# Kernel optimization log

Measured on AMD Instinct MI355X. Metric: run time of the kernel, lower is better.

Reference implementation:

```python
import jax, jax.numpy as jnp
import numpy as np
from jax import lax

WIN = (9, 9, 9)
EPS = 1e-05


def _sum1d(x, axis, win):
    """Sliding-window sum of size `win` along `axis`, zero-padded (SAME)."""
    pad = win // 2
    pads = [(pad, pad) if a == axis else (0, 0) for a in range(x.ndim)]
    xp = jnp.pad(x, pads)
    c = jnp.cumsum(xp, axis=axis)
    c = jnp.pad(c, [(1, 0) if a == axis else (0, 0) for a in range(x.ndim)])
    n = x.shape[axis]
    return (lax.slice_in_dim(c, win, win + n, axis=axis)
            - lax.slice_in_dim(c, 0, n, axis=axis))


def _box_sum(x):
    """Separable 3D box-filter sum == conv3d with ones([9,9,9]), SAME pad."""
    for axis, w in zip((2, 3, 4), WIN):
        x = _sum1d(x, axis, w)
    return x


def setup_inputs() -> dict:
    key = jax.random.key(0)
    k1, k2 = jax.random.split(key)
    shape = (2, 1, 128, 128, 128)
    y_pred = jax.random.normal(k1, shape, dtype=jnp.float32)
    y_true = jax.random.normal(k2, shape, dtype=jnp.float32)
    return {"y_pred": y_pred, "y_true": y_true}


def reference(y_pred, y_true):
    I = y_true.astype(jnp.float32)
    J = y_pred.astype(jnp.float32)
    win_size = float(np.prod(WIN))  # 729

    I_sum = _box_sum(I)
    J_sum = _box_sum(J)
    I2_sum = _box_sum(I * I)
    J2_sum = _box_sum(J * J)
    IJ_sum = _box_sum(I * J)

    u_I = I_sum / win_size
    u_J = J_sum / win_size

    cross = IJ_sum - u_J * I_sum - u_I * J_sum + u_I * u_J * win_size
    I_var = I2_sum - 2 * u_I * I_sum + u_I * u_I * win_size
    J_var = J2_sum - 2 * u_J * J_sum + u_J * u_J * win_size

    cc_map = cross * cross / (I_var * J_var + EPS)
    return jnp.mean(-cc_map)
```

## Files before the change

### kernel.cpp

```cpp
#include <hip/hip_runtime.h>

#define DSZ 128
#define NVOX 4194304.0f

__global__ void ncc_zero(float* out) { out[0] = 0.0f; }

__device__ __forceinline__ float4 f4add(const float4 a, const float4 b) {
    return make_float4(a.x + b.x, a.y + b.y, a.z + b.z, a.w + b.w);
}
__device__ __forceinline__ float4 f4sub(const float4 a, const float4 b) {
    return make_float4(a.x - b.x, a.y - b.y, a.z - b.z, a.w - b.w);
}

__global__ __launch_bounds__(256, 2) void ncc_main(const float* __restrict__ Iin,
                                                   const float* __restrict__ Jin,
                                                   float* __restrict__ out)
{
    const int tx0 = blockIdx.x * 16;
    const int ty0 = blockIdx.y * 32;
    const int b   = blockIdx.z >> 3;
    const int tz0 = (blockIdx.z & 7) * 16;
    const int tid = threadIdx.x;
    const int lx  = tid & 15;
    const int ys  = tid >> 4;

    const float* __restrict__ Ib = Iin + b * (DSZ * DSZ * DSZ);
    const float* __restrict__ Jb = Jin + b * (DSZ * DSZ * DSZ);

    __shared__ float4 s4m[4][40][17];
    __shared__ float  s1v[4][40][24];

    float4 rA4[8], rB4[8];
    float  rA1[8], rB1[8];
#pragma unroll
    for (int i = 0; i < 8; ++i) {
        rA4[i] = make_float4(0.f, 0.f, 0.f, 0.f); rB4[i] = rA4[i];
        rA1[i] = 0.f; rB1[i] = 0.f;
    }
    float4 zA4 = make_float4(0.f, 0.f, 0.f, 0.f), zB4 = zA4;
    float  zA1 = 0.f, zB1 = 0.f;
    float  acc = 0.f;

    auto emit_cc = [&](const float4& z4, const float z1) {
        const float inv = 1.0f / 729.0f;
        const float uI = z4.x * inv;
        const float uJ = z4.y * inv;
        const float cross = z1 - uJ * z4.x - uI * z4.y + uI * uJ * 729.0f;
        const float Ivar  = z4.z - 2.0f * uI * z4.x + uI * uI * 729.0f;
        const float Jvar  = z4.w - 2.0f * uJ * z4.y + uJ * uJ * 729.0f;
        acc += cross * cross / (Ivar * Jvar + 1e-5f);
    };

#pragma unroll 1
    for (int mr = 0; mr < 3; ++mr) {
#pragma unroll
        for (int r4 = 0; r4 < 4; ++r4) {
            const int rnd = 4 * mr + r4;

            for (int t = tid; t < 320; t += 256) {
                const int p   = (t >= 160);
                const int t2  = t - 160 * p;
                const int r   = t2 >> 2;
                const int xg  = t2 & 3;
                const int zp  = tz0 + 2 * rnd + p - 4;
                const int gy  = ty0 + r - 4;
                const int gxb = tx0 + 4 * xg - 4;
                const bool ok = ((unsigned)zp < (unsigned)DSZ) &&
                                ((unsigned)gy < (unsigned)DSZ);
                const int zoff = (zp * DSZ + gy) * DSZ;

                float vi[12], vj[12];
#pragma unroll
                for (int g = 0; g < 3; ++g) {
                    const int gx = gxb + 4 * g;
                    float4 va = make_float4(0.f, 0.f, 0.f, 0.f);
                    float4 vb = va;
                    if (ok && (unsigned)gx < (unsigned)DSZ) {
                        va = *(const float4*)(Ib + zoff + gx);
                        vb = *(const float4*)(Jb + zoff + gx);
                    }
                    vi[4*g+0]=va.x; vi[4*g+1]=va.y; vi[4*g+2]=va.z; vi[4*g+3]=va.w;
                    vj[4*g+0]=vb.x; vj[4*g+1]=vb.y; vj[4*g+2]=vb.z; vj[4*g+3]=vb.w;
                }

                float wI=0.f, wJ=0.f, wII=0.f, wJJ=0.f, wIJ=0.f;
#pragma unroll
                for (int k = 0; k < 9; ++k) {
                    wI += vi[k]; wJ += vj[k];
                    wII = fmaf(vi[k], vi[k], wII);
                    wJJ = fmaf(vj[k], vj[k], wJJ);
                    wIJ = fmaf(vi[k], vj[k], wIJ);
                }
                const int sl = (r4 & 1) * 2 + p;
                float mIJ[4];
                s4m[sl][r][4*xg] = make_float4(wI, wJ, wII, wJJ);
                mIJ[0] = wIJ;
#pragma unroll
                for (int j = 1; j < 4; ++j) {
                    const float ai = vi[8+j], aj = vj[8+j];
                    const float di = vi[j-1], dj = vj[j-1];
                    wI += ai - di; wJ += aj - dj;
                    wII += fmaf(ai, ai, -di * di);
                    wJJ += fmaf(aj, aj, -dj * dj);
                    wIJ += fmaf(ai, aj, -di * dj);
                    s4m[sl][r][4*xg + j] = make_float4(wI, wJ, wII, wJJ);
                    mIJ[j] = wIJ;
                }
                *(float4*)&s1v[sl][r][4*xg] = make_float4(mIJ[0], mIJ[1], mIJ[2], mIJ[3]);
            }
            __syncthreads();

#pragma unroll
            for (int p = 0; p < 2; ++p) {
                const int sl = (r4 & 1) * 2 + p;
                float4 c4 = make_float4(0.f, 0.f, 0.f, 0.f);
                float  c1 = 0.f;
                float4 r0v; float r0s;
#pragma unroll
                for (int dy = 0; dy < 9; ++dy) {
                    const float4 t4 = s4m[sl][2*ys + dy][lx];
                    const float  t1 = s1v[sl][2*ys + dy][lx];
                    if (dy == 0) { r0v = t4; r0s = t1; }
                    c4 = f4add(c4, t4);
                    c1 += t1;
                }
                const float4 r9v = s4m[sl][2*ys + 9][lx];
                const float  r9s = s1v[sl][2*ys + 9][lx];
                const float4 d4 = f4add(f4sub(c4, r0v), r9v);
                const float  d1 = c1 - r0s + r9s;

                const int k = 2 * r4 + p;

                zA4 = f4add(zA4, c4); zA1 += c1;
                if (mr > 0) emit_cc(zA4, zA1);
                zA4 = f4sub(zA4, rA4[k]); zA1 -= rA1[k];
                rA4[k] = c4; rA1[k] = c1;

                zB4 = f4add(zB4, d4); zB1 += d1;
                if (mr > 0) emit_cc(zB4, zB1);
                zB4 = f4sub(zB4, rB4[k]); zB1 -= rB1[k];
                rB4[k] = d4; rB1[k] = d1;
            }
        }
    }

#pragma unroll
    for (int off = 32; off > 0; off >>= 1) acc += __shfl_down(acc, off);
    __shared__ float wpart[4];
    if ((tid & 63) == 0) wpart[tid >> 6] = acc;
    __syncthreads();
    if (tid == 0) {
        const float s = wpart[0] + wpart[1] + wpart[2] + wpart[3];
        atomicAdd(out, s * (-1.0f / NVOX));
    }
}

extern "C" void kernel_launch(void* const* d_in, const int* in_sizes, int n_in,
                              void* d_out, int out_size, void* d_ws, size_t ws_size,
                              hipStream_t stream)
{
    const float* J = (const float*)d_in[0];
    const float* I = (const float*)d_in[1];
    float* out = (float*)d_out;

    ncc_zero<<<dim3(1), dim3(1), 0, stream>>>(out);
    dim3 grid(DSZ / 16, DSZ / 32, 2 * (DSZ / 16));
    ncc_main<<<grid, dim3(256), 0, stream>>>(I, J, out);
}
```

Before: 57.42 us.

## Warp-specialize producer and consumer threads and halve the y tile

Splits each block into overlapping thread roles. Threads 64-255 (192 threads) load and x-reduce the next z-plane pair into shared memory, while threads 0-127 do the y/z window sums and the cc evaluation for the current pair, so loads overlap compute within a round. The y tile shrinks from 32 to 16 rows and the grid doubles, with launch bounds raised to 4 blocks per SU. This trades more halo reloads, from a larger y-halo fraction, for better latency hiding and occupancy. Threads 64-127 run both roles, which serializes their work.

```diff
diff --git a/kernel.cpp b/kernel.cpp
--- a/kernel.cpp
+++ b/kernel.cpp
@@ -12,30 +12,85 @@
     return make_float4(a.x - b.x, a.y - b.y, a.z - b.z, a.w - b.w);
 }
 
-__global__ __launch_bounds__(256, 2) void ncc_main(const float* __restrict__ Iin,
+__global__ __launch_bounds__(256, 4) void ncc_main(const float* __restrict__ Iin,
                                                    const float* __restrict__ Jin,
                                                    float* __restrict__ out)
 {
     const int tx0 = blockIdx.x * 16;
-    const int ty0 = blockIdx.y * 32;
+    const int ty0 = blockIdx.y * 16;
     const int b   = blockIdx.z >> 3;
     const int tz0 = (blockIdx.z & 7) * 16;
     const int tid = threadIdx.x;
-    const int lx  = tid & 15;
-    const int ys  = tid >> 4;
 
     const float* __restrict__ Ib = Iin + b * (DSZ * DSZ * DSZ);
     const float* __restrict__ Jb = Jin + b * (DSZ * DSZ * DSZ);
 
-    __shared__ float4 s4m[4][40][17];
-    __shared__ float  s1v[4][40][24];
+    __shared__ float4 s4m[4][24][17];
+    __shared__ float  s1v[4][24][24];
 
-    float4 rA4[8], rB4[8];
-    float  rA1[8], rB1[8];
+    const bool isB = (tid < 128);
+    const int  lx  = tid & 15;
+    const int  ys  = (tid >> 4) & 7;
+
+    const bool isA = (tid >= 64);
+    const int  ta  = tid - 64;
+    const int  pA  = (ta >= 96) ? 1 : 0;
+    const int  t2  = ta - 96 * pA;
+    const int  rA  = t2 >> 2;
+    const int  xgA = t2 & 3;
+    const int  gyA = ty0 + rA - 4;
+    const int  gxbA = tx0 + 4 * xgA - 4;
+    const bool yokA = ((unsigned)gyA < (unsigned)DSZ);
+
+    auto stageA = [&](const int rnd) {
+        const int zp = tz0 + 2 * rnd + pA - 4;
+        const bool ok = yokA && ((unsigned)zp < (unsigned)DSZ);
+        const int zoff = (zp * DSZ + gyA) * DSZ;
+        float vi[12], vj[12];
+#pragma unroll
+        for (int g = 0; g < 3; ++g) {
+            const int gx = gxbA + 4 * g;
+            float4 va = make_float4(0.f, 0.f, 0.f, 0.f);
+            float4 vb = va;
+            if (ok && (unsigned)gx < (unsigned)DSZ) {
+                va = *(const float4*)(Ib + zoff + gx);
+                vb = *(const float4*)(Jb + zoff + gx);
+            }
+            vi[4*g+0]=va.x; vi[4*g+1]=va.y; vi[4*g+2]=va.z; vi[4*g+3]=va.w;
+            vj[4*g+0]=vb.x; vj[4*g+1]=vb.y; vj[4*g+2]=vb.z; vj[4*g+3]=vb.w;
+        }
+        float wI=0.f, wJ=0.f, wII=0.f, wJJ=0.f, wIJ=0.f;
+#pragma unroll
+        for (int k = 0; k < 9; ++k) {
+            wI += vi[k]; wJ += vj[k];
+            wII = fmaf(vi[k], vi[k], wII);
+            wJJ = fmaf(vj[k], vj[k], wJJ);
+            wIJ = fmaf(vi[k], vj[k], wIJ);
+        }
+        const int sl = (rnd & 1) * 2 + pA;
+        float mIJ[4];
+        s4m[sl][rA][4*xgA] = make_float4(wI, wJ, wII, wJJ);
+        mIJ[0] = wIJ;
+#pragma unroll
+        for (int j = 1; j < 4; ++j) {
+            const float ai = vi[8+j], aj = vj[8+j];
+            const float di = vi[j-1], dj = vj[j-1];
+            wI += ai - di; wJ += aj - dj;
+            wII += fmaf(ai, ai, -di * di);
+            wJJ += fmaf(aj, aj, -dj * dj);
+            wIJ += fmaf(ai, aj, -di * dj);
+            s4m[sl][rA][4*xgA + j] = make_float4(wI, wJ, wII, wJJ);
+            mIJ[j] = wIJ;
+        }
+        *(float4*)&s1v[sl][rA][4*xgA] = make_float4(mIJ[0], mIJ[1], mIJ[2], mIJ[3]);
+    };
+
+    float4 rAv4[8], rBv4[8];
+    float  rAs1[8], rBs1[8];
 #pragma unroll
     for (int i = 0; i < 8; ++i) {
-        rA4[i] = make_float4(0.f, 0.f, 0.f, 0.f); rB4[i] = rA4[i];
-        rA1[i] = 0.f; rB1[i] = 0.f;
+        rAv4[i] = make_float4(0.f, 0.f, 0.f, 0.f); rBv4[i] = rAv4[i];
+        rAs1[i] = 0.f; rBs1[i] = 0.f;
     }
     float4 zA4 = make_float4(0.f, 0.f, 0.f, 0.f), zB4 = zA4;
     float  zA1 = 0.f, zB1 = 0.f;
@@ -51,96 +106,51 @@
         acc += cross * cross / (Ivar * Jvar + 1e-5f);
     };
 
+    if (isA) stageA(0);
+    __syncthreads();
+
 #pragma unroll 1
     for (int mr = 0; mr < 3; ++mr) {
 #pragma unroll
         for (int r4 = 0; r4 < 4; ++r4) {
             const int rnd = 4 * mr + r4;
 
-            for (int t = tid; t < 320; t += 256) {
-                const int p   = (t >= 160);
-                const int t2  = t - 160 * p;
-                const int r   = t2 >> 2;
-                const int xg  = t2 & 3;
-                const int zp  = tz0 + 2 * rnd + p - 4;
-                const int gy  = ty0 + r - 4;
-                const int gxb = tx0 + 4 * xg - 4;
-                const bool ok = ((unsigned)zp < (unsigned)DSZ) &&
-                                ((unsigned)gy < (unsigned)DSZ);
-                const int zoff = (zp * DSZ + gy) * DSZ;
+            if (rnd < 11 && isA) stageA(rnd + 1);
 
-                float vi[12], vj[12];
+            if (isB) {
 #pragma unroll
-                for (int g = 0; g < 3; ++g) {
-                    const int gx = gxb + 4 * g;
-                    float4 va = make_float4(0.f, 0.f, 0.f, 0.f);
-                    float4 vb = va;
-                    if (ok && (unsigned)gx < (unsigned)DSZ) {
-                        va = *(const float4*)(Ib + zoff + gx);
-                        vb = *(const float4*)(Jb + zoff + gx);
+                for (int p = 0; p < 2; ++p) {
+                    const int sl = (r4 & 1) * 2 + p;
+                    float4 c4 = make_float4(0.f, 0.f, 0.f, 0.f);
+                    float  c1 = 0.f;
+                    float4 r0v; float r0s;
+#pragma unroll
+                    for (int dy = 0; dy < 9; ++dy) {
+                        const float4 t4 = s4m[sl][2*ys + dy][lx];
+                        const float  t1 = s1v[sl][2*ys + dy][lx];
+                        if (dy == 0) { r0v = t4; r0s = t1; }
+                        c4 = f4add(c4, t4);
+                        c1 += t1;
                     }
-                    vi[4*g+0]=va.x; vi[4*g+1]=va.y; vi[4*g+2]=va.z; vi[4*g+3]=va.w;
-                    vj[4*g+0]=vb.x; vj[4*g+1]=vb.y; vj[4*g+2]=vb.z; vj[4*g+3]=vb.w;
+                    const float4 r9v = s4m[sl][2*ys + 9][lx];
+                    const float  r9s = s1v[sl][2*ys + 9][lx];
+                    const float4 d4 = f4add(f4sub(c4, r0v), r9v);
+                    const float  d1 = c1 - r0s + r9s;
+
+                    const int k = (2 * r4 + p) & 7;
+
+                    zA4 = f4add(zA4, c4); zA1 += c1;
+                    if (mr > 0) emit_cc(zA4, zA1);
+                    zA4 = f4sub(zA4, rAv4[k]); zA1 -= rAs1[k];
+                    rAv4[k] = c4; rAs1[k] = c1;
+
+                    zB4 = f4add(zB4, d4); zB1 += d1;
+                    if (mr > 0) emit_cc(zB4, zB1);
+                    zB4 = f4sub(zB4, rBv4[k]); zB1 -= rBs1[k];
+                    rBv4[k] = d4; rBs1[k] = d1;
                 }
-
-                float wI=0.f, wJ=0.f, wII=0.f, wJJ=0.f, wIJ=0.f;
-#pragma unroll
-                for (int k = 0; k < 9; ++k) {
-                    wI += vi[k]; wJ += vj[k];
-                    wII = fmaf(vi[k], vi[k], wII);
-                    wJJ = fmaf(vj[k], vj[k], wJJ);
-                    wIJ = fmaf(vi[k], vj[k], wIJ);
-                }
-                const int sl = (r4 & 1) * 2 + p;
-                float mIJ[4];
-                s4m[sl][r][4*xg] = make_float4(wI, wJ, wII, wJJ);
-                mIJ[0] = wIJ;
-#pragma unroll
-                for (int j = 1; j < 4; ++j) {
-                    const float ai = vi[8+j], aj = vj[8+j];
-                    const float di = vi[j-1], dj = vj[j-1];
-                    wI += ai - di; wJ += aj - dj;
-                    wII += fmaf(ai, ai, -di * di);
-                    wJJ += fmaf(aj, aj, -dj * dj);
-                    wIJ += fmaf(ai, aj, -di * dj);
-                    s4m[sl][r][4*xg + j] = make_float4(wI, wJ, wII, wJJ);
-                    mIJ[j] = wIJ;
-                }
-                *(float4*)&s1v[sl][r][4*xg] = make_float4(mIJ[0], mIJ[1], mIJ[2], mIJ[3]);
             }
             __syncthreads();
-
-#pragma unroll
-            for (int p = 0; p < 2; ++p) {
-                const int sl = (r4 & 1) * 2 + p;
-                float4 c4 = make_float4(0.f, 0.f, 0.f, 0.f);
-                float  c1 = 0.f;
-                float4 r0v; float r0s;
-#pragma unroll
-                for (int dy = 0; dy < 9; ++dy) {
-                    const float4 t4 = s4m[sl][2*ys + dy][lx];
-                    const float  t1 = s1v[sl][2*ys + dy][lx];
-                    if (dy == 0) { r0v = t4; r0s = t1; }
-                    c4 = f4add(c4, t4);
-                    c1 += t1;
-                }
-                const float4 r9v = s4m[sl][2*ys + 9][lx];
-                const float  r9s = s1v[sl][2*ys + 9][lx];
-                const float4 d4 = f4add(f4sub(c4, r0v), r9v);
-                const float  d1 = c1 - r0s + r9s;
-
-                const int k = 2 * r4 + p;
-
-                zA4 = f4add(zA4, c4); zA1 += c1;
-                if (mr > 0) emit_cc(zA4, zA1);
-                zA4 = f4sub(zA4, rA4[k]); zA1 -= rA1[k];
-                rA4[k] = c4; rA1[k] = c1;
-
-                zB4 = f4add(zB4, d4); zB1 += d1;
-                if (mr > 0) emit_cc(zB4, zB1);
-                zB4 = f4sub(zB4, rB4[k]); zB1 -= rB1[k];
-                rB4[k] = d4; rB1[k] = d1;
-            }
         }
     }
 
@@ -164,6 +174,6 @@
     float* out = (float*)d_out;
 
     ncc_zero<<<dim3(1), dim3(1), 0, stream>>>(out);
-    dim3 grid(DSZ / 16, DSZ / 32, 2 * (DSZ / 16));
+    dim3 grid(DSZ / 16, DSZ / 16, 2 * (DSZ / 16));
     ncc_main<<<grid, dim3(256), 0, stream>>>(I, J, out);
 }
```

Result: slower. 79.29 us (+38.1%).
